# Performance work log

Measured on AMD Instinct MI355X. Metric: run time of the kernel, lower is better.

The kernel has to match this reference:

```python
import jax, jax.numpy as jnp
import numpy as np

N_WAY = 2
K_SHOT = 5
C = 320
NPTS = 2048
NQ = 2
K_PROTO = 100  # hardcoded k=100 in forward
N_CLS = N_WAY + 1
SIGMA = 1.0
NEG = -1e9


def _l2norm(x, eps=1e-8):
    return x / (jnp.linalg.norm(x, axis=-1, keepdims=True) + eps)


def _class_prototypes(feat, mask, k):
    """Multi-prototype masked pooling for one class.
    feat: [M, C] point features; mask: [M] float (1 = belongs to class).
    Picks k masked seed points, assigns every masked point to its
    nearest (cosine) seed, and returns the k masked cluster means.
    """
    M = feat.shape[0]
    # deterministic seeds: first k masked points (tie-break by index)
    score = mask - jnp.arange(M, dtype=feat.dtype) * 1e-9
    _, seed_idx = jax.lax.top_k(score, k)
    seeds = feat[seed_idx]                      # [k, C]
    sim = _l2norm(feat) @ _l2norm(seeds).T      # [M, k]
    assign = jnp.argmax(sim, axis=1)            # [M]
    onehot = jax.nn.one_hot(assign, k, dtype=feat.dtype) * mask[:, None]  # [M, k]
    num = onehot.T @ feat                       # [k, C]
    den = onehot.sum(axis=0)[:, None] + 1e-8
    return num / den


def _fg_prototypes(support_feat, fg_mask, k):
    # support_feat [n_way, k_shot, C, N] -> per-class point sets [n_way, k_shot*N, C]
    feat = support_feat.transpose(0, 1, 3, 2).reshape(N_WAY, -1, C)
    m = fg_mask.reshape(N_WAY, -1).astype(feat.dtype)
    protos = jax.vmap(lambda f, mm: _class_prototypes(f, mm, k))(feat, m)  # [n_way, k, C]
    labels = jnp.repeat(jnp.arange(1, N_WAY + 1), k)                        # classes 1..n_way
    return protos.reshape(-1, C), jax.nn.one_hot(labels, N_CLS, dtype=feat.dtype)


def _bg_prototypes(support_feat, bg_mask, k):
    feat = support_feat.transpose(0, 1, 3, 2).reshape(-1, C)   # all shots pooled
    m = bg_mask.reshape(-1).astype(feat.dtype)
    protos = _class_prototypes(feat, m, k)                      # [k, C]
    labels = jnp.zeros((k,), dtype=jnp.int32)                   # class 0 = background
    return protos, jax.nn.one_hot(labels, N_CLS, dtype=feat.dtype)


def _predict(prototypes, proto_onehot, qfeat, qlabels):
    # cosine similarity [M, P], per-class max over that class's prototypes
    sim = (_l2norm(qfeat) @ _l2norm(prototypes).T) / SIGMA        # [M, P]
    cls_mask = proto_onehot.T[None] > 0                            # [1, ncls, P]
    pred = jnp.max(jnp.where(cls_mask, sim[:, None, :], NEG), axis=-1)  # [M, ncls]
    logp = jax.nn.log_softmax(pred, axis=-1)
    loss = -jnp.mean(jnp.take_along_axis(logp, qlabels.reshape(-1, 1), axis=1))
    query_pred = pred.reshape(NQ, NPTS, N_CLS).transpose(0, 2, 1)  # [NQ, ncls, NPTS]
    return loss, query_pred


def reference(support_feat, query_feat, support_y, query_y):
    fg_mask = support_y
    bg_mask = 1 - support_y
    fg_protos, fg_labels = _fg_prototypes(support_feat, fg_mask, K_PROTO)
    bg_protos, bg_labels = _bg_prototypes(support_feat, bg_mask, K_PROTO)
    prototypes = jnp.concatenate([bg_protos, fg_protos], axis=0)           # [P, C]
    proto_labels = jnp.concatenate([bg_labels, fg_labels], axis=0)         # [P, ncls]

    qfeat = query_feat.transpose(0, 2, 1).reshape(-1, C)                   # [NQ*NPTS, C]
    loss, query_pred = _predict(prototypes, proto_labels, qfeat, query_y)
    # the forward adds computeCrossEntropyLoss(query_pred, query_y): same CE again
    loss = loss * 2.0

    # post-hoc per-point confidence thresholding (vectorized Python loop)
    qp = jnp.concatenate([query_pred[0], query_pred[1]], axis=-1)          # [ncls, NQ*NPTS]
    predictions = jnp.argmax(qp, axis=0)
    confidences = jnp.max(qp, axis=0)
    final = jnp.where(confidences > jnp.mean(confidences), predictions, -1)
    final_labels = jnp.stack([final[:NPTS], final[NPTS:]], axis=0)         # [2, NPTS]
    return loss, query_pred, final_labels


def setup_inputs() -> dict:
    key = jax.random.key(0)
    k1, k2, k3, k4 = jax.random.split(key, 4)
    return {
        "support_feat": jax.random.normal(k1, (N_WAY, K_SHOT, C, NPTS), dtype=jnp.float32),
        "query_feat": jax.random.normal(k2, (NQ, C, NPTS), dtype=jnp.float32),
        "support_y": jax.random.randint(k3, (N_WAY, K_SHOT, NPTS), 0, 2, dtype=jnp.int32),
        "query_y": jax.random.randint(k4, (NQ, NPTS), 0, 3, dtype=jnp.int32),
    }
```

## Files before the change

### kernel.cpp

```cpp
#include <hip/hip_runtime.h>
#include <math.h>

#define C 320
#define NPTS 2048
#define SUPPTS 20480
#define QPTS 4096
#define KP 100
#define NCLS 3
#define PSTRIDE 300

__global__ __launch_bounds__(64) void k_protoseed(const float* __restrict__ sup,
                                                  const int* __restrict__ sy,
                                                  float* __restrict__ pbufT) {
    int p    = blockIdx.x;
    int lane = threadIdx.x;
    int prob = (p < 100) ? 2 : ((p < 200) ? 0 : 1);
    int rank = (p < 100) ? p : ((p < 200) ? p - 100 : p - 200);
    int M    = (prob == 2) ? SUPPTS : 10240;
    int base = (prob == 1) ? 10240 : 0;
    int found = 0, sp = 0;
    for (int chunk = 0; chunk < M; chunk += 64) {
        int yy = sy[base + chunk + lane];
        int m  = (prob == 2) ? (1 - yy) : yy;
        unsigned long long bal = __ballot(m != 0);
        int cnt = __popcll(bal);
        if (found + cnt > rank) {
            int need = rank - found;
            int prefix = __popcll(bal & ((1ull << lane) - 1ull));
            unsigned long long match = __ballot(m && (prefix == need));
            int pos = __ffsll((unsigned long long)match) - 1;
            sp = base + chunk + pos;
            break;
        }
        found += cnt;
    }
    const float* fb = sup + ((size_t)(sp >> 11) * C) * NPTS + (sp & 2047);
    float v[5]; float s = 0.f;
    #pragma unroll
    for (int i = 0; i < 5; i++) {
        v[i] = fb[(size_t)(lane + i * 64) * NPTS];
        s += v[i] * v[i];
    }
    #pragma unroll
    for (int off = 32; off > 0; off >>= 1) s += __shfl_down(s, off);
    s = __shfl(s, 0);
    float r = 1.0f / (sqrtf(s) + 1e-8f);
    #pragma unroll
    for (int i = 0; i < 5; i++)
        pbufT[(size_t)(lane + i * 64) * PSTRIDE + p] = v[i] * r;
}

__global__ __launch_bounds__(256) void k_assign(const float* __restrict__ sup,
                                                const float* __restrict__ pbT,
                                                float* __restrict__ pmaxv,
                                                int* __restrict__ pmaxj) {
    __shared__ float shp[C * 16];
    __shared__ float red[3 * 64 * 41];
    int b = blockIdx.x, jt = blockIdx.y, tid = threadIdx.x;
    int wave = tid >> 6, lane = tid & 63;
    int prob, pt, gbase, aoff;
    if (b < 40)      { prob = 0; pt = b * 256;        gbase = 0;     aoff = 0; }
    else if (b < 80) { prob = 1; pt = (b - 40) * 256; gbase = 10240; aoff = 10240; }
    else             { prob = 2; pt = (b - 80) * 256; gbase = 0;     aoff = 20480; }
    int j0 = jt * 10;
    int col0 = ((prob == 2) ? 0 : (100 + prob * 100)) + j0;
    for (int i = tid; i < C * 10; i += 256) {
        int j = i % 10, c = i / 10;
        shp[c * 16 + j] = pbT[(size_t)c * PSTRIDE + col0 + j];
    }
    __syncthreads();
    int g = gbase + pt + lane * 4;
    int c0 = wave * 80;
    const float* fb = sup + ((size_t)(g >> 11) * C + c0) * NPTS + (g & 2047);
    float acc[4][10];
    #pragma unroll
    for (int p = 0; p < 4; p++)
        #pragma unroll
        for (int j = 0; j < 10; j++) acc[p][j] = 0.f;
    float4 pf[8];
    #pragma unroll
    for (int k = 0; k < 8; k++) pf[k] = *(const float4*)(fb + (size_t)k * NPTS);
    for (int cc = 0; cc < 80; cc += 8) {
        float4 cur[8];
        #pragma unroll
        for (int k = 0; k < 8; k++) cur[k] = pf[k];
        if (cc + 8 < 80) {
            #pragma unroll
            for (int k = 0; k < 8; k++) pf[k] = *(const float4*)(fb + (size_t)(cc + 8 + k) * NPTS);
        }
        #pragma unroll
        for (int k = 0; k < 8; k++) {
            const float* row = &shp[(c0 + cc + k) * 16];
            float4 p0 = ((const float4*)row)[0];
            float4 p1 = ((const float4*)row)[1];
            float2 p2 = ((const float2*)row)[4];
            float pr[10] = {p0.x,p0.y,p0.z,p0.w,p1.x,p1.y,p1.z,p1.w,p2.x,p2.y};
            float4 cv = cur[k];
            #pragma unroll
            for (int j = 0; j < 10; j++) {
                acc[0][j] += cv.x * pr[j];
                acc[1][j] += cv.y * pr[j];
                acc[2][j] += cv.z * pr[j];
                acc[3][j] += cv.w * pr[j];
            }
        }
    }
    if (wave > 0) {
        float* my = red + ((wave - 1) * 64 + lane) * 41;
        #pragma unroll
        for (int p = 0; p < 4; p++)
            #pragma unroll
            for (int j = 0; j < 10; j++) my[p * 10 + j] = acc[p][j];
    }
    __syncthreads();
    if (wave == 0) {
        #pragma unroll
        for (int w = 0; w < 3; w++) {
            const float* my = red + (w * 64 + lane) * 41;
            #pragma unroll
            for (int p = 0; p < 4; p++)
                #pragma unroll
                for (int j = 0; j < 10; j++) acc[p][j] += my[p * 10 + j];
        }
        size_t base0 = (size_t)(aoff + pt + lane * 4) * 10 + jt;
        #pragma unroll
        for (int p = 0; p < 4; p++) {
            float bv = acc[p][0]; int bj = 0;
            #pragma unroll
            for (int j = 1; j < 10; j++) if (acc[p][j] > bv) { bv = acc[p][j]; bj = j; }
            pmaxv[base0 + (size_t)p * 10] = bv;
            pmaxj[base0 + (size_t)p * 10] = j0 + bj;
        }
    }
}

__global__ __launch_bounds__(256) void k_combine_dst(const float* __restrict__ pmaxv,
                                                     const int* __restrict__ pmaxj,
                                                     const int* __restrict__ sy,
                                                     int* __restrict__ dst,
                                                     float* __restrict__ loss) {
    int g = blockIdx.x * 256 + threadIdx.x;
    if (g == 0) loss[0] = 0.f;
    float bvf = pmaxv[(size_t)g * 10]; int bjf = pmaxj[(size_t)g * 10];
    #pragma unroll
    for (int t = 1; t < 10; t++) {
        float v = pmaxv[(size_t)g * 10 + t];
        if (v > bvf) { bvf = v; bjf = pmaxj[(size_t)g * 10 + t]; }
    }
    size_t gb = (size_t)(SUPPTS + g) * 10;
    float bvb = pmaxv[gb]; int bjb = pmaxj[gb];
    #pragma unroll
    for (int t = 1; t < 10; t++) {
        float v = pmaxv[gb + t];
        if (v > bvb) { bvb = v; bjb = pmaxj[gb + t]; }
    }
    int way = (g >= 10240) ? 1 : 0;
    dst[g] = sy[g] ? (100 + way * 100 + bjf) : bjb;
}

__global__ __launch_bounds__(256) void k_accum_lds(const float* __restrict__ sup,
                                                   const int* __restrict__ dst,
                                                   float* __restrict__ part,
                                                   float* __restrict__ cnt) {
    __shared__ float bins[8 * 200];
    __shared__ float scnt[200];
    int bx = blockIdx.x;
    int ct = blockIdx.y;
    int tid = threadIdx.x;
    int ws = bx >> 1, half = bx & 1;
    int w = (ws >= 5) ? 1 : 0;
    int nbase = half * 1024;
    for (int i = tid; i < 8 * 200; i += 256) bins[i] = 0.f;
    if (ct == 0 && tid < 200) scnt[tid] = 0.f;
    int dreg[4];
    #pragma unroll
    for (int sub = 0; sub < 4; sub++) {
        int d = dst[ws * 2048 + nbase + sub * 256 + tid];
        dreg[sub] = (d < 100) ? d : (d - w * 100);
    }
    __syncthreads();
    if (ct == 0) {
        #pragma unroll
        for (int sub = 0; sub < 4; sub++) atomicAdd(&scnt[dreg[sub]], 1.0f);
    }
    const float* base = sup + ((size_t)ws * C + ct * 8) * NPTS + nbase;
    for (int cl = 0; cl < 8; cl++) {
        const float* row = base + (size_t)cl * NPTS;
        #pragma unroll
        for (int sub = 0; sub < 4; sub++)
            atomicAdd(&bins[cl * 200 + dreg[sub]], row[sub * 256 + tid]);
    }
    __syncthreads();
    float* pout = part + (size_t)(bx * 40 + ct) * 1600;
    for (int i = tid; i < 8 * 200; i += 256) {
        int bin = i >> 3, cl = i & 7;
        pout[i] = bins[cl * 200 + bin];
    }
    if (ct == 0 && tid < 200) cnt[bx * 200 + tid] = scnt[tid];
}

__global__ __launch_bounds__(64) void k_reduce_proto(const float* __restrict__ part,
                                                     const float* __restrict__ cnt,
                                                     float* __restrict__ phatT) {
    int d   = blockIdx.x;
    int tid = threadIdx.x;
    int local, s0, ns;
    if (d < 100)      { local = d;       s0 = 0;  ns = 20; }
    else if (d < 200) { local = d;       s0 = 0;  ns = 10; }
    else              { local = d - 100; s0 = 10; ns = 10; }
    float dn = 0.f;
    for (int k = 0; k < ns; k++) dn += cnt[(s0 + k) * 200 + local];
    float inv = 1.0f / (dn + 1e-8f);
    float vals[5]; float sq = 0.f;
    #pragma unroll
    for (int i = 0; i < 5; i++) {
        int c = tid + i * 64;
        int ct = c >> 3, cl = c & 7;
        float s = 0.f;
        for (int k = 0; k < ns; k++)
            s += part[(size_t)((s0 + k) * 40 + ct) * 1600 + local * 8 + cl];
        float v = s * inv;
        vals[i] = v; sq += v * v;
    }
    #pragma unroll
    for (int off = 32; off > 0; off >>= 1) sq += __shfl_down(sq, off);
    sq = __shfl(sq, 0);
    float rn = 1.0f / (sqrtf(sq) + 1e-8f);
    #pragma unroll
    for (int i = 0; i < 5; i++)
        phatT[(size_t)(tid + i * 64) * PSTRIDE + d] = vals[i] * rn;
}

__global__ __launch_bounds__(256) void k_qpartial(const float* __restrict__ qry,
                                                  const float* __restrict__ phT,
                                                  float* __restrict__ qmaxv,
                                                  float* __restrict__ qrn) {
    __shared__ float shp[C * 16];
    __shared__ float red[3 * 64 * 45];
    int pb = blockIdx.x, jt = blockIdx.y, tid = threadIdx.x;
    int wave = tid >> 6, lane = tid & 63;
    int j0 = jt * 10;
    for (int i = tid; i < C * 10; i += 256) {
        int j = i % 10, c = i / 10;
        shp[c * 16 + j] = phT[(size_t)c * PSTRIDE + j0 + j];
    }
    __syncthreads();
    int m = pb * 256 + lane * 4;
    int c0 = wave * 80;
    const float* fb = qry + ((size_t)(m >> 11) * C + c0) * NPTS + (m & 2047);
    float acc[4][10];
    #pragma unroll
    for (int p = 0; p < 4; p++)
        #pragma unroll
        for (int j = 0; j < 10; j++) acc[p][j] = 0.f;
    float qn[4] = {0.f, 0.f, 0.f, 0.f};
    float4 pf[8];
    #pragma unroll
    for (int k = 0; k < 8; k++) pf[k] = *(const float4*)(fb + (size_t)k * NPTS);
    for (int cc = 0; cc < 80; cc += 8) {
        float4 cur[8];
        #pragma unroll
        for (int k = 0; k < 8; k++) cur[k] = pf[k];
        if (cc + 8 < 80) {
            #pragma unroll
            for (int k = 0; k < 8; k++) pf[k] = *(const float4*)(fb + (size_t)(cc + 8 + k) * NPTS);
        }
        #pragma unroll
        for (int k = 0; k < 8; k++) {
            const float* row = &shp[(c0 + cc + k) * 16];
            float4 p0 = ((const float4*)row)[0];
            float4 p1 = ((const float4*)row)[1];
            float2 p2 = ((const float2*)row)[4];
            float pr[10] = {p0.x,p0.y,p0.z,p0.w,p1.x,p1.y,p1.z,p1.w,p2.x,p2.y};
            float4 cv = cur[k];
            if (jt == 0) {
                qn[0] += cv.x*cv.x; qn[1] += cv.y*cv.y; qn[2] += cv.z*cv.z; qn[3] += cv.w*cv.w;
            }
            #pragma unroll
            for (int j = 0; j < 10; j++) {
                acc[0][j] += cv.x * pr[j];
                acc[1][j] += cv.y * pr[j];
                acc[2][j] += cv.z * pr[j];
                acc[3][j] += cv.w * pr[j];
            }
        }
    }
    if (wave > 0) {
        float* my = red + ((wave - 1) * 64 + lane) * 45;
        #pragma unroll
        for (int p = 0; p < 4; p++)
            #pragma unroll
            for (int j = 0; j < 10; j++) my[p * 10 + j] = acc[p][j];
        #pragma unroll
        for (int p = 0; p < 4; p++) my[40 + p] = qn[p];
    }
    __syncthreads();
    if (wave == 0) {
        #pragma unroll
        for (int w = 0; w < 3; w++) {
            const float* my = red + (w * 64 + lane) * 45;
            #pragma unroll
            for (int p = 0; p < 4; p++)
                #pragma unroll
                for (int j = 0; j < 10; j++) acc[p][j] += my[p * 10 + j];
            #pragma unroll
            for (int p = 0; p < 4; p++) qn[p] += my[40 + p];
        }
        #pragma unroll
        for (int p = 0; p < 4; p++) {
            float bv = acc[p][0];
            #pragma unroll
            for (int j = 1; j < 10; j++) bv = fmaxf(bv, acc[p][j]);
            qmaxv[(size_t)(m + p) * 30 + jt] = bv;
        }
        if (jt == 0) {
            #pragma unroll
            for (int p = 0; p < 4; p++) qrn[m + p] = 1.0f / (sqrtf(qn[p]) + 1e-8f);
        }
    }
}

__global__ __launch_bounds__(256) void k_pred(const float* __restrict__ qmaxv,
                                              const float* __restrict__ qrn,
                                              const int* __restrict__ qy,
                                              float* __restrict__ out,
                                              float* __restrict__ lossacc) {
    int m = blockIdx.x * 256 + threadIdx.x;
    float rn = qrn[m];
    float pred[NCLS];
    #pragma unroll
    for (int cls = 0; cls < NCLS; cls++) {
        float g = qmaxv[(size_t)m * 30 + cls * 10];
        #pragma unroll
        for (int t = 1; t < 10; t++) g = fmaxf(g, qmaxv[(size_t)m * 30 + cls * 10 + t]);
        pred[cls] = rn * g;
    }
    int q = m >> 11, n = m & 2047;
    #pragma unroll
    for (int cls = 0; cls < NCLS; cls++)
        out[1 + ((size_t)(q * NCLS + cls)) * NPTS + n] = pred[cls];
    float mx = fmaxf(pred[0], fmaxf(pred[1], pred[2]));
    float lse = mx + logf(expf(pred[0] - mx) + expf(pred[1] - mx) + expf(pred[2] - mx));
    int lab = qy[m];
    atomicAdd(lossacc, lse - pred[lab]);
}

__global__ __launch_bounds__(1024) void k_final(float* __restrict__ out,
                                                const float* __restrict__ lossacc) {
    __shared__ float red[1024];
    const float* pr = out + 1;
    int tid = threadIdx.x;
    float conf[4]; int lab[4];
    float s = 0.f;
    #pragma unroll
    for (int i = 0; i < 4; i++) {
        int m = tid + i * 1024;
        int q = m >> 11, n = m & 2047;
        float p0 = pr[((size_t)(q * NCLS + 0)) * NPTS + n];
        float p1 = pr[((size_t)(q * NCLS + 1)) * NPTS + n];
        float p2 = pr[((size_t)(q * NCLS + 2)) * NPTS + n];
        int l = 0; float c = p0;
        if (p1 > c) { c = p1; l = 1; }
        if (p2 > c) { c = p2; l = 2; }
        conf[i] = c; lab[i] = l; s += c;
    }
    red[tid] = s; __syncthreads();
    for (int off = 512; off > 0; off >>= 1) {
        if (tid < off) red[tid] += red[tid + off];
        __syncthreads();
    }
    float mean = red[0] / (float)QPTS;
    #pragma unroll
    for (int i = 0; i < 4; i++) {
        int m = tid + i * 1024;
        out[1 + 2 * NCLS * NPTS + m] = (conf[i] > mean) ? (float)lab[i] : -1.0f;
    }
    if (tid == 0) out[0] = 2.0f * lossacc[0] / (float)QPTS;
}

extern "C" void kernel_launch(void* const* d_in, const int* in_sizes, int n_in,
                              void* d_out, int out_size, void* d_ws, size_t ws_size,
                              hipStream_t stream) {
    const float* sup = (const float*)d_in[0];
    const float* qry = (const float*)d_in[1];
    const int*   sy  = (const int*)d_in[2];
    const int*   qy  = (const int*)d_in[3];
    float* out = (float*)d_out;

    float* f      = (float*)d_ws;
    float* qrn    = f;
    float* cnt    = qrn + QPTS;
    float* pbufT  = cnt + 4000;
    float* phatT  = pbufT + 96000;
    float* loss   = phatT + 96000;
    int*   dstb   = (int*)(loss + 4);
    float* trans  = (float*)(dstb + SUPPTS);
    float* pmaxv  = trans;
    int*   pmaxj  = (int*)(pmaxv + 409600);
    float* part   = trans;
    float* qmaxv  = trans;

    k_protoseed<<<300, 64, 0, stream>>>(sup, sy, pbufT);
    {
        dim3 grid(160, 10);
        k_assign<<<grid, 256, 0, stream>>>(sup, pbufT, pmaxv, pmaxj);
    }
    k_combine_dst<<<80, 256, 0, stream>>>(pmaxv, pmaxj, sy, dstb, loss);
    {
        dim3 grid(20, 40);
        k_accum_lds<<<grid, 256, 0, stream>>>(sup, dstb, part, cnt);
    }
    k_reduce_proto<<<300, 64, 0, stream>>>(part, cnt, phatT);
    {
        dim3 grid(16, 30);
        k_qpartial<<<grid, 256, 0, stream>>>(qry, phatT, qmaxv, qrn);
    }
    k_pred<<<16, 256, 0, stream>>>(qmaxv, qrn, qy, out, loss);
    k_final<<<1, 1024, 0, stream>>>(out, loss);
}
```

Before: 246.8 us.

## Restructure assign kernel: full-channel per-thread dot products over 20 prototypes

The nearest-seed assignment kernel now gives each thread 2 points over the whole 320-channel dimension and 20 prototypes, replacing the split-K scheme where 4 waves each summed 80 channels and then reduced through shared memory. This drops the cross-wave LDS reduction and one barrier, and halves the number of prototype tiles (grid y from 10 to 5), so the support features are re-read from global memory half as often. The cost is fewer threads per block (128), narrower float2 loads, 40 accumulators per thread (more register pressure), and a longer serial channel loop per thread. The partial-max buffers and the combine kernel are resized to 5 tiles to match.

```diff
diff --git a/kernel.cpp b/kernel.cpp
--- a/kernel.cpp
+++ b/kernel.cpp
@@ -50,88 +50,66 @@
         pbufT[(size_t)(lane + i * 64) * PSTRIDE + p] = v[i] * r;
 }
 
-__global__ __launch_bounds__(256) void k_assign(const float* __restrict__ sup,
+__global__ __launch_bounds__(128) void k_assign(const float* __restrict__ sup,
                                                 const float* __restrict__ pbT,
                                                 float* __restrict__ pmaxv,
                                                 int* __restrict__ pmaxj) {
-    __shared__ float shp[C * 16];
-    __shared__ float red[3 * 64 * 41];
+    __shared__ float shp[C * 20];
     int b = blockIdx.x, jt = blockIdx.y, tid = threadIdx.x;
-    int wave = tid >> 6, lane = tid & 63;
     int prob, pt, gbase, aoff;
-    if (b < 40)      { prob = 0; pt = b * 256;        gbase = 0;     aoff = 0; }
-    else if (b < 80) { prob = 1; pt = (b - 40) * 256; gbase = 10240; aoff = 10240; }
-    else             { prob = 2; pt = (b - 80) * 256; gbase = 0;     aoff = 20480; }
-    int j0 = jt * 10;
-    int col0 = ((prob == 2) ? 0 : (100 + prob * 100)) + j0;
-    for (int i = tid; i < C * 10; i += 256) {
-        int j = i % 10, c = i / 10;
-        shp[c * 16 + j] = pbT[(size_t)c * PSTRIDE + col0 + j];
-    }
-    __syncthreads();
-    int g = gbase + pt + lane * 4;
-    int c0 = wave * 80;
-    const float* fb = sup + ((size_t)(g >> 11) * C + c0) * NPTS + (g & 2047);
-    float acc[4][10];
-    #pragma unroll
-    for (int p = 0; p < 4; p++)
-        #pragma unroll
-        for (int j = 0; j < 10; j++) acc[p][j] = 0.f;
-    float4 pf[8];
-    #pragma unroll
-    for (int k = 0; k < 8; k++) pf[k] = *(const float4*)(fb + (size_t)k * NPTS);
-    for (int cc = 0; cc < 80; cc += 8) {
-        float4 cur[8];
+    if (b < 40)       { prob = 0; pt = b * 256;         gbase = 0;     aoff = 0; }
+    else if (b < 80)  { prob = 1; pt = (b - 40) * 256;  gbase = 10240; aoff = 10240; }
+    else              { prob = 2; pt = (b - 80) * 256;  gbase = 0;     aoff = 20480; }
+    int j0 = jt * 20;
+    int col0 = (prob == 2) ? 0 : (100 + prob * 100);
+    for (int i = tid; i < C * 20; i += 128) {
+        int j = i % 20, c = i / 20;
+        shp[i] = pbT[(size_t)c * PSTRIDE + col0 + j0 + j];
+    }
+    __syncthreads();
+    int g = gbase + pt + tid * 2;
+    const float* fb = sup + ((size_t)(g >> 11) * C) * NPTS + (g & 2047);
+    float acc0[20], acc1[20];
+    #pragma unroll
+    for (int j = 0; j < 20; j++) { acc0[j] = 0.f; acc1[j] = 0.f; }
+    float2 pf[8];
+    #pragma unroll
+    for (int k = 0; k < 8; k++) pf[k] = *(const float2*)(fb + (size_t)k * NPTS);
+    for (int cc = 0; cc < C; cc += 8) {
+        float2 cur[8];
         #pragma unroll
         for (int k = 0; k < 8; k++) cur[k] = pf[k];
-        if (cc + 8 < 80) {
-            #pragma unroll
-            for (int k = 0; k < 8; k++) pf[k] = *(const float4*)(fb + (size_t)(cc + 8 + k) * NPTS);
+        if (cc + 8 < C) {
+            #pragma unroll
+            for (int k = 0; k < 8; k++) pf[k] = *(const float2*)(fb + (size_t)(cc + 8 + k) * NPTS);
         }
         #pragma unroll
         for (int k = 0; k < 8; k++) {
-            const float* row = &shp[(c0 + cc + k) * 16];
-            float4 p0 = ((const float4*)row)[0];
-            float4 p1 = ((const float4*)row)[1];
-            float2 p2 = ((const float2*)row)[4];
-            float pr[10] = {p0.x,p0.y,p0.z,p0.w,p1.x,p1.y,p1.z,p1.w,p2.x,p2.y};
-            float4 cv = cur[k];
-            #pragma unroll
-            for (int j = 0; j < 10; j++) {
-                acc[0][j] += cv.x * pr[j];
-                acc[1][j] += cv.y * pr[j];
-                acc[2][j] += cv.z * pr[j];
-                acc[3][j] += cv.w * pr[j];
-            }
-        }
-    }
-    if (wave > 0) {
-        float* my = red + ((wave - 1) * 64 + lane) * 41;
-        #pragma unroll
-        for (int p = 0; p < 4; p++)
-            #pragma unroll
-            for (int j = 0; j < 10; j++) my[p * 10 + j] = acc[p][j];
-    }
-    __syncthreads();
-    if (wave == 0) {
-        #pragma unroll
-        for (int w = 0; w < 3; w++) {
-            const float* my = red + (w * 64 + lane) * 41;
-            #pragma unroll
-            for (int p = 0; p < 4; p++)
-                #pragma unroll
-                for (int j = 0; j < 10; j++) acc[p][j] += my[p * 10 + j];
-        }
-        size_t base0 = (size_t)(aoff + pt + lane * 4) * 10 + jt;
-        #pragma unroll
-        for (int p = 0; p < 4; p++) {
-            float bv = acc[p][0]; int bj = 0;
-            #pragma unroll
-            for (int j = 1; j < 10; j++) if (acc[p][j] > bv) { bv = acc[p][j]; bj = j; }
-            pmaxv[base0 + (size_t)p * 10] = bv;
-            pmaxj[base0 + (size_t)p * 10] = j0 + bj;
-        }
-    }
+            const float4* r = (const float4*)&shp[(cc + k) * 20];
+            float4 a = r[0], d1 = r[1], d2 = r[2], d3 = r[3], d4 = r[4];
+            float px = cur[k].x, py = cur[k].y;
+            acc0[0]+=px*a.x;  acc1[0]+=py*a.x;  acc0[1]+=px*a.y;  acc1[1]+=py*a.y;
+            acc0[2]+=px*a.z;  acc1[2]+=py*a.z;  acc0[3]+=px*a.w;  acc1[3]+=py*a.w;
+            acc0[4]+=px*d1.x; acc1[4]+=py*d1.x; acc0[5]+=px*d1.y; acc1[5]+=py*d1.y;
+            acc0[6]+=px*d1.z; acc1[6]+=py*d1.z; acc0[7]+=px*d1.w; acc1[7]+=py*d1.w;
+            acc0[8]+=px*d2.x; acc1[8]+=py*d2.x; acc0[9]+=px*d2.y; acc1[9]+=py*d2.y;
+            acc0[10]+=px*d2.z;acc1[10]+=py*d2.z;acc0[11]+=px*d2.w;acc1[11]+=py*d2.w;
+            acc0[12]+=px*d3.x;acc1[12]+=py*d3.x;acc0[13]+=px*d3.y;acc1[13]+=py*d3.y;
+            acc0[14]+=px*d3.z;acc1[14]+=py*d3.z;acc0[15]+=px*d3.w;acc1[15]+=py*d3.w;
+            acc0[16]+=px*d4.x;acc1[16]+=py*d4.x;acc0[17]+=px*d4.y;acc1[17]+=py*d4.y;
+            acc0[18]+=px*d4.z;acc1[18]+=py*d4.z;acc0[19]+=px*d4.w;acc1[19]+=py*d4.w;
+        }
+    }
+    float bv0 = acc0[0]; int bj0 = 0;
+    float bv1 = acc1[0]; int bj1 = 0;
+    #pragma unroll
+    for (int j = 1; j < 20; j++) {
+        if (acc0[j] > bv0) { bv0 = acc0[j]; bj0 = j; }
+        if (acc1[j] > bv1) { bv1 = acc1[j]; bj1 = j; }
+    }
+    size_t a0 = (size_t)(aoff + pt + tid * 2) * 5 + jt;
+    pmaxv[a0]     = bv0; pmaxj[a0]     = j0 + bj0;
+    pmaxv[a0 + 5] = bv1; pmaxj[a0 + 5] = j0 + bj1;
 }
 
 __global__ __launch_bounds__(256) void k_combine_dst(const float* __restrict__ pmaxv,
@@ -141,16 +119,16 @@
                                                      float* __restrict__ loss) {
     int g = blockIdx.x * 256 + threadIdx.x;
     if (g == 0) loss[0] = 0.f;
-    float bvf = pmaxv[(size_t)g * 10]; int bjf = pmaxj[(size_t)g * 10];
-    #pragma unroll
-    for (int t = 1; t < 10; t++) {
-        float v = pmaxv[(size_t)g * 10 + t];
-        if (v > bvf) { bvf = v; bjf = pmaxj[(size_t)g * 10 + t]; }
-    }
-    size_t gb = (size_t)(SUPPTS + g) * 10;
+    float bvf = pmaxv[(size_t)g * 5]; int bjf = pmaxj[(size_t)g * 5];
+    #pragma unroll
+    for (int t = 1; t < 5; t++) {
+        float v = pmaxv[(size_t)g * 5 + t];
+        if (v > bvf) { bvf = v; bjf = pmaxj[(size_t)g * 5 + t]; }
+    }
+    size_t gb = (size_t)(SUPPTS + g) * 5;
     float bvb = pmaxv[gb]; int bjb = pmaxj[gb];
     #pragma unroll
-    for (int t = 1; t < 10; t++) {
+    for (int t = 1; t < 5; t++) {
         float v = pmaxv[gb + t];
         if (v > bvb) { bvb = v; bjb = pmaxj[gb + t]; }
     }
@@ -396,14 +374,14 @@
     int*   dstb   = (int*)(loss + 4);
     float* trans  = (float*)(dstb + SUPPTS);
     float* pmaxv  = trans;
-    int*   pmaxj  = (int*)(pmaxv + 409600);
+    int*   pmaxj  = (int*)(pmaxv + 204800);
     float* part   = trans;
     float* qmaxv  = trans;
 
     k_protoseed<<<300, 64, 0, stream>>>(sup, sy, pbufT);
     {
-        dim3 grid(160, 10);
-        k_assign<<<grid, 256, 0, stream>>>(sup, pbufT, pmaxv, pmaxj);
+        dim3 grid(160, 5);
+        k_assign<<<grid, 128, 0, stream>>>(sup, pbufT, pmaxv, pmaxj);
     }
     k_combine_dst<<<80, 256, 0, stream>>>(pmaxv, pmaxj, sy, dstb, loss);
     {
```

Result: faster. 237.5 us (-3.8%).

## Use single-wave k_assign blocks with 8 points per thread over the full channel range

Applied to the files above, without the earlier changes.

Restructures the assignment kernel so each 64-thread block handles 512 points, with every thread covering 8 points across all 320 channels. This removes the split of channels over four waves and the shared-memory cross-wave reduction. Global loads are double-buffered in two register sets. The cost is 80 accumulators per thread, which adds register pressure, and far fewer threads in flight (800 single-wave blocks), which may hurt latency hiding.

```diff
diff --git a/kernel.cpp b/kernel.cpp
--- a/kernel.cpp
+++ b/kernel.cpp
@@ -50,87 +50,88 @@
         pbufT[(size_t)(lane + i * 64) * PSTRIDE + p] = v[i] * r;
 }
 
-__global__ __launch_bounds__(256) void k_assign(const float* __restrict__ sup,
-                                                const float* __restrict__ pbT,
-                                                float* __restrict__ pmaxv,
-                                                int* __restrict__ pmaxj) {
+__global__ __launch_bounds__(64) void k_assign(const float* __restrict__ sup,
+                                               const float* __restrict__ pbT,
+                                               float* __restrict__ pmaxv,
+                                               int* __restrict__ pmaxj) {
     __shared__ float shp[C * 16];
-    __shared__ float red[3 * 64 * 41];
-    int b = blockIdx.x, jt = blockIdx.y, tid = threadIdx.x;
-    int wave = tid >> 6, lane = tid & 63;
+    int b = blockIdx.x, jt = blockIdx.y, lane = threadIdx.x;
     int prob, pt, gbase, aoff;
-    if (b < 40)      { prob = 0; pt = b * 256;        gbase = 0;     aoff = 0; }
-    else if (b < 80) { prob = 1; pt = (b - 40) * 256; gbase = 10240; aoff = 10240; }
-    else             { prob = 2; pt = (b - 80) * 256; gbase = 0;     aoff = 20480; }
+    if (b < 20)      { prob = 0; pt = b * 512;        gbase = 0;     aoff = 0; }
+    else if (b < 40) { prob = 1; pt = (b - 20) * 512; gbase = 10240; aoff = 10240; }
+    else             { prob = 2; pt = (b - 40) * 512; gbase = 0;     aoff = 20480; }
     int j0 = jt * 10;
     int col0 = ((prob == 2) ? 0 : (100 + prob * 100)) + j0;
-    for (int i = tid; i < C * 10; i += 256) {
+    for (int i = lane; i < C * 10; i += 64) {
         int j = i % 10, c = i / 10;
         shp[c * 16 + j] = pbT[(size_t)c * PSTRIDE + col0 + j];
     }
     __syncthreads();
-    int g = gbase + pt + lane * 4;
-    int c0 = wave * 80;
-    const float* fb = sup + ((size_t)(g >> 11) * C + c0) * NPTS + (g & 2047);
-    float acc[4][10];
-    #pragma unroll
-    for (int p = 0; p < 4; p++)
+    int g = gbase + pt + lane * 8;
+    const float* fb = sup + ((size_t)(g >> 11) * C) * NPTS + (g & 2047);
+    float acc[8][10];
+    #pragma unroll
+    for (int p = 0; p < 8; p++)
         #pragma unroll
         for (int j = 0; j < 10; j++) acc[p][j] = 0.f;
-    float4 pf[8];
-    #pragma unroll
-    for (int k = 0; k < 8; k++) pf[k] = *(const float4*)(fb + (size_t)k * NPTS);
-    for (int cc = 0; cc < 80; cc += 8) {
-        float4 cur[8];
-        #pragma unroll
-        for (int k = 0; k < 8; k++) cur[k] = pf[k];
-        if (cc + 8 < 80) {
-            #pragma unroll
-            for (int k = 0; k < 8; k++) pf[k] = *(const float4*)(fb + (size_t)(cc + 8 + k) * NPTS);
-        }
-        #pragma unroll
-        for (int k = 0; k < 8; k++) {
-            const float* row = &shp[(c0 + cc + k) * 16];
-            float4 p0 = ((const float4*)row)[0];
-            float4 p1 = ((const float4*)row)[1];
-            float2 p2 = ((const float2*)row)[4];
-            float pr[10] = {p0.x,p0.y,p0.z,p0.w,p1.x,p1.y,p1.z,p1.w,p2.x,p2.y};
-            float4 cv = cur[k];
-            #pragma unroll
-            for (int j = 0; j < 10; j++) {
-                acc[0][j] += cv.x * pr[j];
-                acc[1][j] += cv.y * pr[j];
-                acc[2][j] += cv.z * pr[j];
-                acc[3][j] += cv.w * pr[j];
+    float4 bufA[8], bufB[8];
+    #pragma unroll
+    for (int k = 0; k < 4; k++) {
+        bufA[2*k]   = *(const float4*)(fb + (size_t)k * NPTS);
+        bufA[2*k+1] = *(const float4*)(fb + (size_t)k * NPTS + 4);
+    }
+    for (int cc = 0; cc < C; cc += 8) {
+        #pragma unroll
+        for (int k = 0; k < 4; k++) {
+            int c = cc + 4 + k;
+            bufB[2*k]   = *(const float4*)(fb + (size_t)c * NPTS);
+            bufB[2*k+1] = *(const float4*)(fb + (size_t)c * NPTS + 4);
+        }
+        #pragma unroll
+        for (int k = 0; k < 4; k++) {
+            const float* row = &shp[(cc + k) * 16];
+            float4 q0 = ((const float4*)row)[0];
+            float4 q1 = ((const float4*)row)[1];
+            float2 q2 = ((const float2*)row)[4];
+            float pr[10] = {q0.x,q0.y,q0.z,q0.w,q1.x,q1.y,q1.z,q1.w,q2.x,q2.y};
+            float4 lo = bufA[2*k], hi = bufA[2*k+1];
+            float pv[8] = {lo.x,lo.y,lo.z,lo.w,hi.x,hi.y,hi.z,hi.w};
+            #pragma unroll
+            for (int p = 0; p < 8; p++)
+                #pragma unroll
+                for (int j = 0; j < 10; j++) acc[p][j] += pv[p] * pr[j];
+        }
+        if (cc + 8 < C) {
+            #pragma unroll
+            for (int k = 0; k < 4; k++) {
+                int c = cc + 8 + k;
+                bufA[2*k]   = *(const float4*)(fb + (size_t)c * NPTS);
+                bufA[2*k+1] = *(const float4*)(fb + (size_t)c * NPTS + 4);
             }
         }
-    }
-    if (wave > 0) {
-        float* my = red + ((wave - 1) * 64 + lane) * 41;
-        #pragma unroll
-        for (int p = 0; p < 4; p++)
-            #pragma unroll
-            for (int j = 0; j < 10; j++) my[p * 10 + j] = acc[p][j];
-    }
-    __syncthreads();
-    if (wave == 0) {
-        #pragma unroll
-        for (int w = 0; w < 3; w++) {
-            const float* my = red + (w * 64 + lane) * 41;
-            #pragma unroll
-            for (int p = 0; p < 4; p++)
+        #pragma unroll
+        for (int k = 0; k < 4; k++) {
+            const float* row = &shp[(cc + 4 + k) * 16];
+            float4 q0 = ((const float4*)row)[0];
+            float4 q1 = ((const float4*)row)[1];
+            float2 q2 = ((const float2*)row)[4];
+            float pr[10] = {q0.x,q0.y,q0.z,q0.w,q1.x,q1.y,q1.z,q1.w,q2.x,q2.y};
+            float4 lo = bufB[2*k], hi = bufB[2*k+1];
+            float pv[8] = {lo.x,lo.y,lo.z,lo.w,hi.x,hi.y,hi.z,hi.w};
+            #pragma unroll
+            for (int p = 0; p < 8; p++)
                 #pragma unroll
-                for (int j = 0; j < 10; j++) acc[p][j] += my[p * 10 + j];
-        }
-        size_t base0 = (size_t)(aoff + pt + lane * 4) * 10 + jt;
-        #pragma unroll
-        for (int p = 0; p < 4; p++) {
-            float bv = acc[p][0]; int bj = 0;
-            #pragma unroll
-            for (int j = 1; j < 10; j++) if (acc[p][j] > bv) { bv = acc[p][j]; bj = j; }
-            pmaxv[base0 + (size_t)p * 10] = bv;
-            pmaxj[base0 + (size_t)p * 10] = j0 + bj;
-        }
+                for (int j = 0; j < 10; j++) acc[p][j] += pv[p] * pr[j];
+        }
+    }
+    size_t base0 = (size_t)(aoff + pt + lane * 8) * 10 + jt;
+    #pragma unroll
+    for (int p = 0; p < 8; p++) {
+        float bv = acc[p][0]; int bj = 0;
+        #pragma unroll
+        for (int j = 1; j < 10; j++) if (acc[p][j] > bv) { bv = acc[p][j]; bj = j; }
+        pmaxv[base0 + (size_t)p * 10] = bv;
+        pmaxj[base0 + (size_t)p * 10] = j0 + bj;
     }
 }
 
@@ -402,8 +403,8 @@
 
     k_protoseed<<<300, 64, 0, stream>>>(sup, sy, pbufT);
     {
-        dim3 grid(160, 10);
-        k_assign<<<grid, 256, 0, stream>>>(sup, pbufT, pmaxv, pmaxj);
+        dim3 grid(80, 10);
+        k_assign<<<grid, 64, 0, stream>>>(sup, pbufT, pmaxv, pmaxj);
     }
     k_combine_dst<<<80, 256, 0, stream>>>(pmaxv, pmaxj, sy, dstb, loss);
     {
```

Result: no change. 242.0 us (-2.0%).
